# Kernel optimization log

Measured on AMD Instinct MI355X. Metric: run time of the kernel, lower is better.

## Reference

```python
import jax, jax.numpy as jnp
import numpy as np

N = 100000        # nodes
E = 1600000       # edges (avg degree 16)
F_IN = 128        # num_node_features
H = 64            # hidden_channels
F_EDGE = 8        # num_edge_features (output dim per edge)


def setup_inputs() -> dict:
    key = jax.random.key(0)
    ks = jax.random.split(key, 9)
    x = jax.random.normal(ks[0], (N, F_IN), dtype=jnp.float32)
    edge_index = jax.random.randint(ks[1], (2, E), 0, N, dtype=jnp.int32)
    s = 0.05
    W1 = jax.random.normal(ks[2], (F_IN, H), jnp.float32) * s
    b1 = jnp.zeros((H,), jnp.float32)
    W2 = jax.random.normal(ks[3], (H, H), jnp.float32) * s
    b2 = jnp.zeros((H,), jnp.float32)
    Wl = jax.random.normal(ks[4], (2 * H, F_EDGE), jnp.float32) * s
    bl = jnp.zeros((F_EDGE,), jnp.float32)
    return {"x": x, "edge_index": edge_index,
            "W1": W1, "b1": b1, "W2": W2, "b2": b2, "Wl": Wl, "bl": bl}


def gcn_conv(x, W, b, row, col, n):
    # GCNConv: h = D^{-1/2} (A + I) D^{-1/2} (x W) + b
    h = x @ W
    sl = jnp.arange(n, dtype=row.dtype)          # self-loops
    r = jnp.concatenate([row, sl])
    c = jnp.concatenate([col, sl])
    ones = jnp.ones(r.shape[0], dtype=h.dtype)
    deg = jax.ops.segment_sum(ones, c, num_segments=n)      # in-degree incl. self-loop
    dinv = jax.lax.rsqrt(jnp.maximum(deg, 1e-12))
    norm = dinv[r] * dinv[c]                                 # symmetric normalization
    agg = jax.ops.segment_sum(norm[:, None] * h[r], c, num_segments=n)
    return agg + b


def reference(x, edge_index, W1, b1, W2, b2, Wl, bl):
    row, col = edge_index[0], edge_index[1]
    h = jax.nn.relu(gcn_conv(x, W1, b1, row, col, N))
    # dropout p=0.5 is identity at inference (training=False)
    h = jax.nn.relu(gcn_conv(h, W2, b2, row, col, N))
    x_i = h[row]                                  # [E, H]
    x_j = h[col]                                  # [E, H]
    return jnp.concatenate([x_i, x_j], axis=-1) @ Wl + bl   # [E, F_EDGE]
```

## Files before the change

kernel.cpp:

```cpp
#include <hip/hip_runtime.h>
#include <hip/hip_bf16.h>

static constexpr int NN  = 100000;
static constexpr int NE  = 1600000;
static constexpr int FIN = 128;
static constexpr int HD  = 64;

static constexpr int NB    = 256;
static constexpr int NPB   = 392;
static constexpr int EPB   = NE / NB;
static constexpr unsigned long long DIV392_MAGIC = 43826197ULL;

static constexpr int NSL = 4;

typedef __attribute__((ext_vector_type(8))) short bf16x8;
typedef __attribute__((ext_vector_type(4))) float f32x4;

__device__ __forceinline__ float bf2f(unsigned short u) {
    return __uint_as_float(((unsigned int)u) << 16);
}
__device__ __forceinline__ unsigned short f2bf(float f) {
    __hip_bfloat16 hb = __float2bfloat16(f);
    return *(unsigned short*)&hb;
}
__device__ __forceinline__ int bucket_of(int c) {
    return (int)(((unsigned long long)(unsigned int)c * DIV392_MAGIC) >> 34);
}

__device__ __forceinline__ float load_in(const void* p, size_t i, int isbf) {
    return isbf ? bf2f(((const unsigned short*)p)[i]) : ((const float*)p)[i];
}

__global__ __launch_bounds__(256) void k_hist(const int* __restrict__ col, int* __restrict__ hist,
                                              const unsigned short* __restrict__ xu,
                                              int* __restrict__ flag) {
    __shared__ int h[4][NB];
    int t = threadIdx.x, w = t >> 6;
#pragma unroll
    for (int r = 0; r < 4; ++r) h[r][t] = 0;
    __syncthreads();
    int base = blockIdx.x * EPB;
    for (int e = base + t; e < base + EPB; e += 256)
        atomicAdd(&h[w][bucket_of(col[e])], 1);
    __syncthreads();
    hist[t * NB + blockIdx.x] = h[0][t] + h[1][t] + h[2][t] + h[3][t];
    if (blockIdx.x == 0) {
        __syncthreads();
        int cnt = 0;
        for (int k = t; k < 4096; k += 256) {
            unsigned short u = xu[2 * k];
            int ex = (u >> 7) & 0xFF;
            cnt += (ex >= 110 && ex <= 135) ? 1 : 0;
        }
        h[0][t] = cnt;
        __syncthreads();
        for (int off = 128; off > 0; off >>= 1) {
            if (t < off) h[0][t] += h[0][t + off];
            __syncthreads();
        }
        if (t == 0) flag[0] = (h[0][0] >= 2048) ? 1 : 0;
    }
}

__global__ __launch_bounds__(256) void k_gscan1(int* __restrict__ a, int* __restrict__ bsums) {
    __shared__ int sd[256];
    int t = threadIdx.x;
    int base = blockIdx.x * 1024 + t * 4;
    int v0 = a[base], v1 = a[base + 1], v2 = a[base + 2], v3 = a[base + 3];
    int tsum = v0 + v1 + v2 + v3;
    sd[t] = tsum;
    __syncthreads();
    for (int off = 1; off < 256; off <<= 1) {
        int tmp = (t >= off) ? sd[t - off] : 0;
        __syncthreads();
        sd[t] += tmp;
        __syncthreads();
    }
    int run = sd[t] - tsum;
    a[base] = run; run += v0;
    a[base + 1] = run; run += v1;
    a[base + 2] = run; run += v2;
    a[base + 3] = run;
    if (t == 255) bsums[blockIdx.x] = sd[t];
}

__device__ __forceinline__ void scan_bsums(const int* __restrict__ bsumsRaw, int* sb) {
    int t = threadIdx.x;
    int myv = 0;
    if (t < 64) { myv = bsumsRaw[t]; sb[t] = myv; }
    __syncthreads();
    for (int off = 1; off < 64; off <<= 1) {
        int v = (t < 64 && t >= off) ? sb[t - off] : 0;
        __syncthreads();
        if (t < 64) sb[t] += v;
        __syncthreads();
    }
    if (t < 64) sb[t] -= myv;
    __syncthreads();
}

__global__ __launch_bounds__(256) void k_binfill(const int* __restrict__ row, const int* __restrict__ col,
                                                 const int* __restrict__ histS,
                                                 const int* __restrict__ bsumsRaw,
                                                 int* __restrict__ csr_tmp) {
    __shared__ int cur[NB];
    __shared__ int sb[64];
    int t = threadIdx.x;
    scan_bsums(bsumsRaw, sb);
    cur[t] = histS[t * NB + blockIdx.x] + sb[t >> 2];
    __syncthreads();
    int base = blockIdx.x * EPB;
    for (int e = base + t; e < base + EPB; e += 256) {
        int r = row[e], c = col[e];
        int b = bucket_of(c);
        int p = atomicAdd(&cur[b], 1);
        csr_tmp[p] = r | ((c - b * NPB) << 17);
    }
}

__global__ __launch_bounds__(256) void k_bsort(const int* __restrict__ csr_tmp,
                                               const int* __restrict__ histS,
                                               const int* __restrict__ bsumsRaw,
                                               int* __restrict__ csr_src,
                                               int* __restrict__ start,
                                               float* __restrict__ dinv) {
    __shared__ int cnt[512];
    __shared__ int cur[512];
    __shared__ int sb[64];
    int t = threadIdx.x;
    int k = blockIdx.x;
    cnt[t] = 0; cnt[t + 256] = 0;
    scan_bsums(bsumsRaw, sb);
    int S = histS[k * NB] + sb[k >> 2];
    int E = (k < NB - 1) ? (histS[(k + 1) * NB] + sb[(k + 1) >> 2]) : NE;
    int nbase = k * NPB;
    __syncthreads();
    for (int e = S + t; e < E; e += 256)
        atomicAdd(&cnt[csr_tmp[e] >> 17], 1);
    __syncthreads();
    int rc0 = cnt[t], rc1 = cnt[t + 256];
    for (int d = 1; d < 512; d <<= 1) {
        int idx = (t + 1) * (d << 1) - 1;
        if (idx < 512) cnt[idx] += cnt[idx - d];
        __syncthreads();
    }
    if (t == 0) cnt[511] = 0;
    __syncthreads();
    for (int d = 256; d >= 1; d >>= 1) {
        int idx = (t + 1) * (d << 1) - 1;
        if (idx < 512) { int tmp = cnt[idx - d]; cnt[idx - d] = cnt[idx]; cnt[idx] += tmp; }
        __syncthreads();
    }
    int n0 = nbase + t;
    if (n0 < NN) {
        start[n0] = S + cnt[t] + rc0;
        dinv[n0] = rsqrtf((float)(rc0 + 1));
    }
    int li = t + 256;
    int n1 = nbase + li;
    if (li < NPB && n1 < NN) {
        start[n1] = S + cnt[li] + rc1;
        dinv[n1] = rsqrtf((float)(rc1 + 1));
    }
    cur[t] = cnt[t]; cur[t + 256] = cnt[t + 256];
    __syncthreads();
    for (int e = S + t; e < E; e += 256) {
        int u = csr_tmp[e];
        int p = atomicAdd(&cur[u >> 17], 1);
        csr_src[S + p] = u & 0x1FFFF;
    }
}

template <int K, bool XDUAL>
__global__ __launch_bounds__(256) void k_gemm_mfma(const void* __restrict__ X,
                                                   const void* __restrict__ W,
                                                   const float* __restrict__ dinv,
                                                   unsigned short* __restrict__ T4,
                                                   const int* __restrict__ flag) {
    constexpr int KT = K / 32;
    __shared__ unsigned short Bs[KT * 4 * 64 * 8];
    int isbf = flag[0];
    for (int tup = threadIdx.x; tup < KT * 4 * 64; tup += 256) {
        int l  = tup & 63;
        int nt = (tup >> 6) & 3;
        int kt = tup >> 8;
        int n  = nt * 16 + (l & 15);
        int kb = kt * 32 + (l >> 4) * 8;
        unsigned short tmp[8];
#pragma unroll
        for (int j = 0; j < 8; ++j) tmp[j] = f2bf(load_in(W, (size_t)(kb + j) * HD + n, isbf));
        *((uint4*)&Bs[(size_t)tup * 8]) = *((const uint4*)tmp);
    }
    __syncthreads();
    int wave = threadIdx.x >> 6, lane = threadIdx.x & 63;
    int quad = lane >> 4, m = lane & 15;
    int row0 = blockIdx.x * 64 + wave * 16;
    int row  = row0 + m;
    int rowc = (row < NN) ? row : (NN - 1);
    bool xf32 = XDUAL && (isbf == 0);
    const char* xrow = (const char*)X + (size_t)rowc * K * (xf32 ? 4 : 2);
    f32x4 acc[4];
#pragma unroll
    for (int nt = 0; nt < 4; ++nt) acc[nt] = (f32x4){0.f, 0.f, 0.f, 0.f};
#pragma unroll
    for (int kt = 0; kt < KT; ++kt) {
        bf16x8 a;
        if (!xf32) {
            a = *((const bf16x8*)(xrow + (size_t)(kt * 32 + quad * 8) * 2));
        } else {
            const float4* fp = (const float4*)(xrow + (size_t)(kt * 32 + quad * 8) * 4);
            float4 u0 = fp[0], u1 = fp[1];
            unsigned short tmp[8] = {f2bf(u0.x), f2bf(u0.y), f2bf(u0.z), f2bf(u0.w),
                                     f2bf(u1.x), f2bf(u1.y), f2bf(u1.z), f2bf(u1.w)};
            a = *((const bf16x8*)tmp);
        }
#pragma unroll
        for (int nt = 0; nt < 4; ++nt) {
            bf16x8 b = *((const bf16x8*)&Bs[(size_t)((kt * 4 + nt) * 64 + lane) * 8]);
            acc[nt] = __builtin_amdgcn_mfma_f32_16x16x32_bf16(a, b, acc[nt], 0, 0, 0);
        }
    }
#pragma unroll
    for (int r = 0; r < 4; ++r) {
        int orow = row0 + quad * 4 + r;
        if (orow < NN) {
            float sc = dinv[orow];
#pragma unroll
            for (int nt = 0; nt < 4; ++nt)
                T4[((size_t)nt * NN + orow) * 16 + m] = f2bf(acc[nt][r] * sc);
        }
    }
}

__global__ __launch_bounds__(256) void k_agg4(const unsigned short* __restrict__ T4,
                                              const int* __restrict__ endOff,
                                              const int* __restrict__ csr_src,
                                              const float* __restrict__ dinv,
                                              const void* __restrict__ bias,
                                              const int* __restrict__ flag,
                                              unsigned short* __restrict__ H4) {
    int isbf = flag[0];
    int slice = blockIdx.x & 3;
    int grp   = blockIdx.x >> 2;
    int t = threadIdx.x;
    int li   = t >> 3;
    int slot = (t >> 1) & 3;
    int fl   = (t & 1) * 8;
    int i = grp * 32 + li;
    int end = endOff[i];
    int beg = (i == 0) ? 0 : endOff[i - 1];
    const unsigned short* Ts = T4 + (size_t)slice * NN * 16;
    union U { uint4 u; unsigned short s[8]; };
    float a[8];
#pragma unroll
    for (int j = 0; j < 8; ++j) a[j] = 0.f;
    int k = beg + slot;
    int sA = (k < end) ? csr_src[k] : -1;
    int sB = (k + 4 < end) ? csr_src[k + 4] : -1;
    while (sA >= 0) {
        U rA, rB;
        rA.u = *((const uint4*)(Ts + (size_t)sA * 16 + fl));
        bool hb = (sB >= 0);
        if (hb) rB.u = *((const uint4*)(Ts + (size_t)sB * 16 + fl));
        k += 8;
        sA = (k < end) ? csr_src[k] : -1;
        sB = (k + 4 < end) ? csr_src[k + 4] : -1;
#pragma unroll
        for (int j = 0; j < 8; ++j) a[j] += bf2f(rA.s[j]);
        if (hb) {
#pragma unroll
            for (int j = 0; j < 8; ++j) a[j] += bf2f(rB.s[j]);
        }
    }
#pragma unroll
    for (int j = 0; j < 8; ++j) {
        a[j] += __shfl_xor(a[j], 2, 64);
        a[j] += __shfl_xor(a[j], 4, 64);
    }
    U sf; sf.u = *((const uint4*)(Ts + (size_t)i * 16 + fl));
    float di = dinv[i];
    U o;
#pragma unroll
    for (int j = 0; j < 8; ++j) {
        float v = a[j] + bf2f(sf.s[j]);
        float b = load_in(bias, (size_t)(slice * 16 + fl + j), isbf);
        o.s[j] = f2bf(fmaxf(fmaf(di, v, b), 0.f));
    }
    if (slot == 0)
        *((uint4*)(H4 + ((size_t)slice * NN + i) * 16 + fl)) = o.u;
}

__global__ __launch_bounds__(256) void k_gemm_h(const unsigned short* __restrict__ H4,
                                                const void* __restrict__ W,
                                                const float* __restrict__ dinv,
                                                unsigned short* __restrict__ Tb4,
                                                const int* __restrict__ flag) {
    __shared__ unsigned short Bs[2 * 4 * 64 * 8];
    int isbf = flag[0];
    for (int tup = threadIdx.x; tup < 512; tup += 256) {
        int l  = tup & 63;
        int nt = (tup >> 6) & 3;
        int kt = tup >> 8;
        int n  = nt * 16 + (l & 15);
        int kb = kt * 32 + (l >> 4) * 8;
        unsigned short tmp[8];
#pragma unroll
        for (int j = 0; j < 8; ++j) tmp[j] = f2bf(load_in(W, (size_t)(kb + j) * HD + n, isbf));
        *((uint4*)&Bs[(size_t)tup * 8]) = *((const uint4*)tmp);
    }
    __syncthreads();
    int wave = threadIdx.x >> 6, lane = threadIdx.x & 63;
    int quad = lane >> 4, m = lane & 15;
    int row0 = blockIdx.x * 64 + wave * 16;
    int row  = row0 + m;
    int rowc = (row < NN) ? row : (NN - 1);
    f32x4 acc[4];
#pragma unroll
    for (int nt = 0; nt < 4; ++nt) acc[nt] = (f32x4){0.f, 0.f, 0.f, 0.f};
#pragma unroll
    for (int kt = 0; kt < 2; ++kt) {
        int k0 = kt * 32 + quad * 8;
        bf16x8 a = *((const bf16x8*)&H4[((size_t)(k0 >> 4) * NN + rowc) * 16 + (k0 & 15)]);
#pragma unroll
        for (int nt = 0; nt < 4; ++nt) {
            bf16x8 b = *((const bf16x8*)&Bs[(size_t)((kt * 4 + nt) * 64 + lane) * 8]);
            acc[nt] = __builtin_amdgcn_mfma_f32_16x16x32_bf16(a, b, acc[nt], 0, 0, 0);
        }
    }
#pragma unroll
    for (int r = 0; r < 4; ++r) {
        int orow = row0 + quad * 4 + r;
        if (orow < NN) {
            float sc = dinv[orow];
#pragma unroll
            for (int nt = 0; nt < 4; ++nt)
                Tb4[((size_t)nt * NN + orow) * 16 + m] = f2bf(acc[nt][r] * sc);
        }
    }
}

__global__ __launch_bounds__(256) void k_pgemm_h(const unsigned short* __restrict__ H4,
                                                 const void* __restrict__ Wl,
                                                 const void* __restrict__ bl,
                                                 unsigned short* __restrict__ P,
                                                 const int* __restrict__ flag) {
    int isbf = flag[0];
    int wave = threadIdx.x >> 6, lane = threadIdx.x & 63;
    int quad = lane >> 4, m = lane & 15;
    bf16x8 bfr[2];
#pragma unroll
    for (int kt = 0; kt < 2; ++kt) {
        unsigned short tmp[8];
#pragma unroll
        for (int j = 0; j < 8; ++j) {
            int kk = kt * 32 + quad * 8 + j;
            float w = (m < 8) ? load_in(Wl, (size_t)kk * 8 + m, isbf)
                              : load_in(Wl, (size_t)(64 + kk) * 8 + (m - 8), isbf);
            tmp[j] = f2bf(w);
        }
        bfr[kt] = *((const bf16x8*)tmp);
    }
    float binit = (m < 8) ? load_in(bl, m, isbf) : 0.f;
    int row0 = blockIdx.x * 64 + wave * 16;
    int row  = row0 + m;
    int rowc = (row < NN) ? row : (NN - 1);
    f32x4 acc = (f32x4){binit, binit, binit, binit};
#pragma unroll
    for (int kt = 0; kt < 2; ++kt) {
        int k0 = kt * 32 + quad * 8;
        bf16x8 a = *((const bf16x8*)&H4[((size_t)(k0 >> 4) * NN + rowc) * 16 + (k0 & 15)]);
        acc = __builtin_amdgcn_mfma_f32_16x16x32_bf16(a, bfr[kt], acc, 0, 0, 0);
    }
#pragma unroll
    for (int r = 0; r < 4; ++r) {
        int orow = row0 + quad * 4 + r;
        if (orow < NN) P[(size_t)orow * 16 + m] = f2bf(acc[r]);
    }
}

__global__ __launch_bounds__(256) void k_edge_add(const unsigned short* __restrict__ P,
                                                  const int* __restrict__ erow,
                                                  const int* __restrict__ ecol,
                                                  void* __restrict__ out,
                                                  const int* __restrict__ flag) {
    int isbf = flag[0];
    int e = blockIdx.x * 256 + threadIdx.x;
    int i = erow[e], j = ecol[e];
    ushort4 r0 = *((const ushort4*)(P + (size_t)i * 16));
    ushort4 r1 = *((const ushort4*)(P + (size_t)i * 16 + 4));
    ushort4 c0 = *((const ushort4*)(P + (size_t)j * 16 + 8));
    ushort4 c1 = *((const ushort4*)(P + (size_t)j * 16 + 12));
    float v[8] = {bf2f(r0.x) + bf2f(c0.x), bf2f(r0.y) + bf2f(c0.y),
                  bf2f(r0.z) + bf2f(c0.z), bf2f(r0.w) + bf2f(c0.w),
                  bf2f(r1.x) + bf2f(c1.x), bf2f(r1.y) + bf2f(c1.y),
                  bf2f(r1.z) + bf2f(c1.z), bf2f(r1.w) + bf2f(c1.w)};
    if (isbf) {
        union { unsigned short h[8]; uint4 u; } p;
#pragma unroll
        for (int o = 0; o < 8; ++o) p.h[o] = f2bf(v[o]);
        *((uint4*)((__hip_bfloat16*)out + (size_t)e * 8)) = p.u;
    } else {
        float* op = (float*)out + (size_t)e * 8;
        ((float4*)op)[0] = make_float4(v[0], v[1], v[2], v[3]);
        ((float4*)op)[1] = make_float4(v[4], v[5], v[6], v[7]);
    }
}

extern "C" void kernel_launch(void* const* d_in, const int* in_sizes, int n_in,
                              void* d_out, int out_size, void* d_ws, size_t ws_size,
                              hipStream_t stream) {
    const void* x  = d_in[0];
    const int*  ei = (const int*)d_in[1];
    const void* W1 = d_in[2];
    const void* b1 = d_in[3];
    const void* W2 = d_in[4];
    const void* b2 = d_in[5];
    const void* Wl = d_in[6];
    const void* bl = d_in[7];
    const int* row = ei;
    const int* col = ei + NE;

    char* ws = (char*)d_ws;
    int*   flag    = (int*)ws;    ws += 16;
    int*   hist    = (int*)ws;    ws += (size_t)NB * NB * 4;
    int*   bsums   = (int*)ws;    ws += 256 * 4;
    int*   start   = (int*)ws;    ws += (size_t)NN * 4;
    float* dinv    = (float*)ws;  ws += (size_t)NN * 4;
    int*   csr_tmp = (int*)ws;    ws += (size_t)NE * 4;
    int*   csr_src = (int*)ws;    ws += (size_t)NE * 4;
    unsigned short* T4  = (unsigned short*)ws;  ws += (size_t)NN * 64 * 2;
    unsigned short* H4  = (unsigned short*)ws;  ws += (size_t)NN * 64 * 2;
    unsigned short* Tb4 = (unsigned short*)ws;  ws += (size_t)NN * 64 * 2;
    unsigned short* P   = (unsigned short*)ws;

    int gE   = (NE + 255) / 256;
    int gN64 = (NN + 63) / 64;
    int gAgg = (NN / 32) * NSL;

    k_hist   <<<NB, 256, 0, stream>>>(col, hist, (const unsigned short*)x, flag);
    k_gscan1 <<<64, 256, 0, stream>>>(hist, bsums);
    k_binfill<<<NB, 256, 0, stream>>>(row, col, hist, bsums, csr_tmp);
    k_bsort  <<<NB, 256, 0, stream>>>(csr_tmp, hist, bsums, csr_src, start, dinv);

    k_gemm_mfma<FIN, true><<<gN64, 256, 0, stream>>>(x, W1, dinv, T4, flag);
    k_agg4 <<<gAgg, 256, 0, stream>>>(T4, start, csr_src, dinv, b1, flag, H4);

    k_gemm_h<<<gN64, 256, 0, stream>>>(H4, W2, dinv, Tb4, flag);
    k_agg4 <<<gAgg, 256, 0, stream>>>(Tb4, start, csr_src, dinv, b2, flag, H4);

    k_pgemm_h<<<gN64, 256, 0, stream>>>(H4, Wl, bl, P, flag);
    k_edge_add<<<gE, 256, 0, stream>>>(P, row, col, d_out, flag);
}
```

Baseline: 299.5 us.

## Stage CSR neighbor indices in shared memory and widen per-thread gather in aggregation

The aggregation kernel now handles 64 nodes per block instead of 32. Each block cooperatively loads its nodes' end offsets and contiguous CSR source indices into LDS, falling back to global reads if the edge count exceeds capacity. Each node uses 4 threads (2 slots) instead of 8. Each thread issues four independent 16-byte gathers per iteration, which should give more memory-level parallelism and remove dependent index loads from the gather loop. The costs are two block barriers and fewer threads per node, which could lengthen the per-node loops for high-degree nodes.

```diff
diff --git a/kernel.cpp b/kernel.cpp
--- a/kernel.cpp
+++ b/kernel.cpp
@@ -12,6 +12,9 @@
 static constexpr unsigned long long DIV392_MAGIC = 43826197ULL;
 
 static constexpr int NSL = 4;
+
+static constexpr int AGN  = 64;
+static constexpr int ACAP = 1536;
 
 typedef __attribute__((ext_vector_type(8))) short bf16x8;
 typedef __attribute__((ext_vector_type(4))) float f32x4;
@@ -239,55 +242,90 @@
                                               const void* __restrict__ bias,
                                               const int* __restrict__ flag,
                                               unsigned short* __restrict__ H4) {
+    __shared__ int sIdx[ACAP];
+    __shared__ int sEnd[AGN + 1];
     int isbf = flag[0];
     int slice = blockIdx.x & 3;
     int grp   = blockIdx.x >> 2;
+    int i0 = grp * AGN;
     int t = threadIdx.x;
-    int li   = t >> 3;
-    int slot = (t >> 1) & 3;
+    if (t <= AGN) {
+        int n = i0 + t - 1;
+        sEnd[t] = (n < 0) ? 0 : endOff[(n < NN) ? n : (NN - 1)];
+    }
+    __syncthreads();
+    int base  = sEnd[0];
+    int total = sEnd[AGN] - base;
+    bool fast = (total <= ACAP);
+    if (fast)
+        for (int k = t; k < total; k += 256) sIdx[k] = csr_src[base + k];
+    __syncthreads();
+    int li   = t >> 2;
+    int slot = (t >> 1) & 1;
     int fl   = (t & 1) * 8;
-    int i = grp * 32 + li;
-    int end = endOff[i];
-    int beg = (i == 0) ? 0 : endOff[i - 1];
+    int i    = i0 + li;
     const unsigned short* Ts = T4 + (size_t)slice * NN * 16;
     union U { uint4 u; unsigned short s[8]; };
     float a[8];
 #pragma unroll
     for (int j = 0; j < 8; ++j) a[j] = 0.f;
-    int k = beg + slot;
-    int sA = (k < end) ? csr_src[k] : -1;
-    int sB = (k + 4 < end) ? csr_src[k + 4] : -1;
-    while (sA >= 0) {
-        U rA, rB;
-        rA.u = *((const uint4*)(Ts + (size_t)sA * 16 + fl));
-        bool hb = (sB >= 0);
-        if (hb) rB.u = *((const uint4*)(Ts + (size_t)sB * 16 + fl));
-        k += 8;
-        sA = (k < end) ? csr_src[k] : -1;
-        sB = (k + 4 < end) ? csr_src[k + 4] : -1;
-#pragma unroll
-        for (int j = 0; j < 8; ++j) a[j] += bf2f(rA.s[j]);
-        if (hb) {
-#pragma unroll
-            for (int j = 0; j < 8; ++j) a[j] += bf2f(rB.s[j]);
-        }
-    }
-#pragma unroll
-    for (int j = 0; j < 8; ++j) {
-        a[j] += __shfl_xor(a[j], 2, 64);
-        a[j] += __shfl_xor(a[j], 4, 64);
-    }
-    U sf; sf.u = *((const uint4*)(Ts + (size_t)i * 16 + fl));
-    float di = dinv[i];
-    U o;
-#pragma unroll
-    for (int j = 0; j < 8; ++j) {
-        float v = a[j] + bf2f(sf.s[j]);
-        float b = load_in(bias, (size_t)(slice * 16 + fl + j), isbf);
-        o.s[j] = f2bf(fmaxf(fmaf(di, v, b), 0.f));
-    }
-    if (slot == 0)
+    if (i < NN) {
+        int beg = sEnd[li] - base;
+        int end = sEnd[li + 1] - base;
+        int k = beg + slot;
+        if (fast) {
+            for (; k + 6 < end; k += 8) {
+                int s0 = sIdx[k], s1 = sIdx[k + 2], s2 = sIdx[k + 4], s3 = sIdx[k + 6];
+                U t0, t1, t2, t3;
+                t0.u = *((const uint4*)(Ts + (size_t)s0 * 16 + fl));
+                t1.u = *((const uint4*)(Ts + (size_t)s1 * 16 + fl));
+                t2.u = *((const uint4*)(Ts + (size_t)s2 * 16 + fl));
+                t3.u = *((const uint4*)(Ts + (size_t)s3 * 16 + fl));
+#pragma unroll
+                for (int j = 0; j < 8; ++j)
+                    a[j] += bf2f(t0.s[j]) + bf2f(t1.s[j]) + bf2f(t2.s[j]) + bf2f(t3.s[j]);
+            }
+            for (; k < end; k += 2) {
+                int s = sIdx[k];
+                U tv; tv.u = *((const uint4*)(Ts + (size_t)s * 16 + fl));
+#pragma unroll
+                for (int j = 0; j < 8; ++j) a[j] += bf2f(tv.s[j]);
+            }
+        } else {
+            for (; k + 6 < end; k += 8) {
+                int s0 = csr_src[base + k],     s1 = csr_src[base + k + 2];
+                int s2 = csr_src[base + k + 4], s3 = csr_src[base + k + 6];
+                U t0, t1, t2, t3;
+                t0.u = *((const uint4*)(Ts + (size_t)s0 * 16 + fl));
+                t1.u = *((const uint4*)(Ts + (size_t)s1 * 16 + fl));
+                t2.u = *((const uint4*)(Ts + (size_t)s2 * 16 + fl));
+                t3.u = *((const uint4*)(Ts + (size_t)s3 * 16 + fl));
+#pragma unroll
+                for (int j = 0; j < 8; ++j)
+                    a[j] += bf2f(t0.s[j]) + bf2f(t1.s[j]) + bf2f(t2.s[j]) + bf2f(t3.s[j]);
+            }
+            for (; k < end; k += 2) {
+                int s = csr_src[base + k];
+                U tv; tv.u = *((const uint4*)(Ts + (size_t)s * 16 + fl));
+#pragma unroll
+                for (int j = 0; j < 8; ++j) a[j] += bf2f(tv.s[j]);
+            }
+        }
+    }
+#pragma unroll
+    for (int j = 0; j < 8; ++j) a[j] += __shfl_xor(a[j], 2, 64);
+    if (i < NN && slot == 0) {
+        float di = dinv[i];
+        U sf; sf.u = *((const uint4*)(Ts + (size_t)i * 16 + fl));
+        U o;
+#pragma unroll
+        for (int j = 0; j < 8; ++j) {
+            float v = a[j] + bf2f(sf.s[j]);
+            float b = load_in(bias, (size_t)(slice * 16 + fl + j), isbf);
+            o.s[j] = f2bf(fmaxf(fmaf(di, v, b), 0.f));
+        }
         *((uint4*)(H4 + ((size_t)slice * NN + i) * 16 + fl)) = o.u;
+    }
 }
 
 __global__ __launch_bounds__(256) void k_gemm_h(const unsigned short* __restrict__ H4,
@@ -435,7 +473,7 @@
 
     int gE   = (NE + 255) / 256;
     int gN64 = (NN + 63) / 64;
-    int gAgg = (NN / 32) * NSL;
+    int gAgg = ((NN + AGN - 1) / AGN) * NSL;
 
     k_hist   <<<NB, 256, 0, stream>>>(col, hist, (const unsigned short*)x, flag);
     k_gscan1 <<<64, 256, 0, stream>>>(hist, bsums);
```

Result: faster. 289.2 us (-3.4%).
